# Optimization experiments

Measured on AMD Instinct MI355X. Metric: run time of the kernel, lower is better.

Reference implementation:

```python
import jax, jax.numpy as jnp
import numpy as np

N, E, M = 8192, 32768, 2048
D, H1, C = 768, 8, 768
NEG_SLOPE = 0.2


def gat_conv(x, src, dst, W, att_src, att_dst, bias, heads, out_ch):
    # PyG GATConv (eval mode, concat=True, add_self_loops already applied to src/dst)
    n = x.shape[0]
    h = (x @ W).reshape(n, heads, out_ch)                      # [N,H,C]
    a_src = jnp.einsum('nhc,hc->nh', h, att_src)               # [N,H]
    a_dst = jnp.einsum('nhc,hc->nh', h, att_dst)
    e = jax.nn.leaky_relu(a_src[src] + a_dst[dst], NEG_SLOPE)  # [E',H]
    # softmax over incoming edges of each dst node
    m = jax.ops.segment_max(e, dst, num_segments=n)
    e = jnp.exp(e - m[dst])
    denom = jax.ops.segment_sum(e, dst, num_segments=n)
    alpha = e / (denom[dst] + 1e-16)                           # [E',H]
    msg = h[src] * alpha[:, :, None]                           # [E',H,C]
    out = jax.ops.segment_sum(msg, dst, num_segments=n)        # [N,H,C]
    return out.reshape(n, heads * out_ch) + bias


def setup_inputs() -> dict:
    key = jax.random.key(0)
    ks = jax.random.split(key, 16)
    s = 0.02
    inp = {
        'x': jax.random.normal(ks[0], (N, D), jnp.float32),
        'edge_index': jax.random.randint(ks[1], (2, E), 0, N, jnp.int64),
        'mask_idx': jax.random.randint(ks[2], (M,), 0, N, jnp.int64),
        'W1': jax.random.normal(ks[3], (D, H1 * C), jnp.float32) * s,
        'att_src1': jax.random.normal(ks[4], (H1, C), jnp.float32) * s,
        'att_dst1': jax.random.normal(ks[5], (H1, C), jnp.float32) * s,
        'b1': jnp.zeros((H1 * C,), jnp.float32),
        'W2': jax.random.normal(ks[6], (H1 * C, C), jnp.float32) * s,
        'att_src2': jax.random.normal(ks[7], (1, C), jnp.float32) * s,
        'att_dst2': jax.random.normal(ks[8], (1, C), jnp.float32) * s,
        'b2': jnp.zeros((C,), jnp.float32),
        # fc: 1536 -> 768, classifier: 768 -> 2
        'fc_w': jax.random.normal(ks[9], (2 * C, C), jnp.float32) * s,
        'fc_b': jnp.zeros((C,), jnp.float32),
        'cls_w': jax.random.normal(ks[10], (C, 2), jnp.float32) * s,
        'cls_b': jnp.zeros((2,), jnp.float32),
    }
    return inp


def reference(x, edge_index, mask_idx, W1, att_src1, att_dst1, b1,
              W2, att_src2, att_dst2, b2, fc_w, fc_b, cls_w, cls_b):
    n = x.shape[0]
    loops = jnp.arange(n, dtype=edge_index.dtype)
    src = jnp.concatenate([edge_index[0], loops])   # PyG default add_self_loops
    dst = jnp.concatenate([edge_index[1], loops])
    h = gat_conv(x, src, dst, W1, att_src1, att_dst1, b1, H1, C)   # [N, 6144]
    h = jax.nn.elu(h)
    h = gat_conv(h, src, dst, W2, att_src2, att_dst2, b2, 1, C)    # [N, 768]
    x_gemb = h[mask_idx]                                           # [M, 768]
    x_emb = x[mask_idx]                                            # [M, 768]
    out = jnp.concatenate([x_gemb, x_emb], axis=1) @ fc_w + fc_b   # [M, 768]
    out = out @ cls_w + cls_b                                      # [M, 2]
    return out
```

## Files before the change

kernel.cpp:

```cpp
#include <hip/hip_runtime.h>

typedef unsigned short ushort_t;
typedef __attribute__((ext_vector_type(8))) __bf16 bf16x8;
typedef __attribute__((ext_vector_type(8))) unsigned short ushort8;
typedef __attribute__((ext_vector_type(4))) unsigned short ushort4v;
typedef __attribute__((ext_vector_type(4))) float f32x4;

#define N_NODES 8192
#define NODE_MASK 8191
#define E_EDGES 32768
#define E_TOT   40960
#define M_MASK  2048
#define D_IN    768
#define C_CH    768
#define F1      6144

typedef __attribute__((address_space(1))) const void* gas_ptr;
typedef __attribute__((address_space(3))) void* las_ptr;

__device__ __forceinline__ float bf2f(ushort_t u) {
    union { unsigned int i; float f; } v; v.i = ((unsigned int)u) << 16; return v.f;
}
__device__ __forceinline__ ushort_t f2bf(float f) {
    union { float f; unsigned int i; } v; v.f = f;
    unsigned int r = v.i + 0x7fffu + ((v.i >> 16) & 1u);
    return (ushort_t)(r >> 16);
}

__global__ void init_kernel(int* deg, int* fill, int* flags) {
    int i = blockIdx.x * 256 + threadIdx.x;
    if (i < N_NODES) { deg[i] = 0; fill[i] = 0; }
    if (i < 2) flags[i] = 0;
}
__global__ void detect_kernel(const int* __restrict__ raw, int nhalf, int* __restrict__ flag) {
    int i = blockIdx.x * 256 + threadIdx.x;
    if (i < nhalf && raw[2 * i + 1] != 0) atomicOr(flag, 1);
}
__global__ void convert_idx_kernel(const void* __restrict__ raw, int n,
                                   const int* __restrict__ flag, int* __restrict__ out) {
    int i = blockIdx.x * 256 + threadIdx.x;
    if (i >= n) return;
    int v = (*flag) ? ((const int*)raw)[i] : (int)((const long long*)raw)[i];
    out[i] = v & NODE_MASK;
}

__global__ void cvt_bf16_kernel(const float* __restrict__ in, ushort_t* __restrict__ out, int n4) {
    int i = blockIdx.x * 256 + threadIdx.x;
    if (i >= n4) return;
    f32x4 v = *(const f32x4*)(in + i * 4);
    ushort_t o0 = f2bf(v[0]), o1 = f2bf(v[1]), o2 = f2bf(v[2]), o3 = f2bf(v[3]);
    unsigned long long pk = (unsigned long long)o0 | ((unsigned long long)o1 << 16)
                          | ((unsigned long long)o2 << 32) | ((unsigned long long)o3 << 48);
    *(unsigned long long*)(out + i * 4) = pk;
}

__global__ __launch_bounds__(256) void transpose_cvt_kernel(
    const float* __restrict__ in, ushort_t* __restrict__ out, int R, int Ccols)
{
    __shared__ ushort_t tile[32][33];
    int tx = threadIdx.x & 31, ty = threadIdx.x >> 5;
    int x  = blockIdx.x * 32 + tx;
    int y0 = blockIdx.y * 32;
#pragma unroll
    for (int i = 0; i < 4; ++i)
        tile[ty + i * 8][tx] = f2bf(in[(size_t)(y0 + ty + i * 8) * Ccols + x]);
    __syncthreads();
#pragma unroll
    for (int i = 0; i < 4; ++i)
        out[(size_t)(blockIdx.x * 32 + ty + i * 8) * R + y0 + tx] = tile[tx][ty + i * 8];
}

__global__ __launch_bounds__(256) void gemm_bt_kernel(
    const ushort_t* __restrict__ A, const ushort_t* __restrict__ Bt,
    ushort_t* __restrict__ C, const float* __restrict__ bias,
    float* __restrict__ Cp,
    int M, int N, int K, int k0, int ksz)
{
    __shared__ ushort_t lsA[128 * 64];
    __shared__ ushort_t lsB[128 * 64];

    const int tid  = threadIdx.x;
    const int lane = tid & 63;
    const int wave = tid >> 6;
    const int wm = wave >> 1, wn = wave & 1;

    const int GX = gridDim.x, GY = gridDim.y;
    const int lin = blockIdx.y * GX + blockIdx.x;
    const int byg = (GY >= 8) ? (GY >> 3) : 1;
    const int xcd = lin & 7;
    const int jj  = lin >> 3;
    const int bx  = (GY >= 8) ? (jj / byg) : blockIdx.x;
    const int by  = (GY >= 8) ? (xcd * byg + (jj % byg)) : blockIdx.y;

    const f32x4 zero = {0.f, 0.f, 0.f, 0.f};
    f32x4 acc[4][4];
#pragma unroll
    for (int i = 0; i < 4; ++i)
#pragma unroll
        for (int j = 0; j < 4; ++j) acc[i][j] = zero;

    const int l8 = lane >> 3;
    const int c8 = lane & 7;
    const int q  = lane >> 4;
    const int rl = lane & 15;

    const int kbeg = k0 + blockIdx.z * ksz;
    for (int kt = kbeg; kt < kbeg + ksz; kt += 64) {
        __syncthreads();
#pragma unroll
        for (int i = 0; i < 4; ++i) {
            int rbase = wave * 32 + i * 8;
            int row   = rbase + l8;
            int gch   = c8 ^ (row & 7);
            const ushort_t* gA = A  + (size_t)(by * 128 + row) * K + kt + gch * 8;
            const ushort_t* gB = Bt + (size_t)(bx * 128 + row) * K + kt + gch * 8;
            __builtin_amdgcn_global_load_lds((gas_ptr)gA, (las_ptr)(lsA + rbase * 64), 16, 0, 0);
            __builtin_amdgcn_global_load_lds((gas_ptr)gB, (las_ptr)(lsB + rbase * 64), 16, 0, 0);
        }
        __syncthreads();
#pragma unroll
        for (int s = 0; s < 2; ++s) {
            bf16x8 af[4], bfv[4];
#pragma unroll
            for (int i = 0; i < 4; ++i) {
                int Ra = wm * 64 + i * 16 + rl;
                af[i]  = *(const bf16x8*)(lsA + Ra * 64 + (((s * 4 + q) ^ (Ra & 7)) * 8));
                int Rb = wn * 64 + i * 16 + rl;
                bfv[i] = *(const bf16x8*)(lsB + Rb * 64 + (((s * 4 + q) ^ (Rb & 7)) * 8));
            }
#pragma unroll
            for (int i = 0; i < 4; ++i)
#pragma unroll
                for (int j = 0; j < 4; ++j)
                    acc[i][j] = __builtin_amdgcn_mfma_f32_16x16x32_bf16(af[i], bfv[j], acc[i][j], 0, 0, 0);
        }
    }
    if (Cp) {
        float* Cpz = Cp + (size_t)blockIdx.z * M * N;
#pragma unroll
        for (int j = 0; j < 4; ++j) {
            int col = bx * 128 + wn * 64 + j * 16 + rl;
#pragma unroll
            for (int i = 0; i < 4; ++i)
#pragma unroll
                for (int t = 0; t < 4; ++t) {
                    int row = by * 128 + wm * 64 + i * 16 + q * 4 + t;
                    Cpz[(size_t)row * N + col] = acc[i][j][t];
                }
        }
    } else {
#pragma unroll
        for (int j = 0; j < 4; ++j) {
            int col = bx * 128 + wn * 64 + j * 16 + rl;
            float bv = bias ? bias[col] : 0.0f;
#pragma unroll
            for (int i = 0; i < 4; ++i)
#pragma unroll
                for (int t = 0; t < 4; ++t) {
                    int row = by * 128 + wm * 64 + i * 16 + q * 4 + t;
                    C[(size_t)row * N + col] = f2bf(acc[i][j][t] + bv);
                }
        }
    }
}

__global__ void indeg_kernel(const int* __restrict__ eic, int* __restrict__ deg) {
    int e = blockIdx.x * 256 + threadIdx.x;
    if (e >= E_TOT) return;
    int dst = (e < E_EDGES) ? eic[E_EDGES + e] : (e - E_EDGES);
    atomicAdd(&deg[dst], 1);
}
__global__ __launch_bounds__(256) void scan_kernel(const int* __restrict__ deg, int* __restrict__ rowptr) {
    __shared__ int part[256];
    int t = threadIdx.x;
    int local[32];
    int s = 0;
#pragma unroll
    for (int i = 0; i < 32; ++i) { local[i] = deg[t * 32 + i]; s += local[i]; }
    part[t] = s;
    __syncthreads();
    for (int off = 1; off < 256; off <<= 1) {
        int v = (t >= off) ? part[t - off] : 0;
        __syncthreads();
        part[t] += v;
        __syncthreads();
    }
    int run = (t == 0) ? 0 : part[t - 1];
#pragma unroll
    for (int i = 0; i < 32; ++i) { rowptr[t * 32 + i] = run; run += local[i]; }
    if (t == 255) rowptr[N_NODES] = run;
}
__global__ void scatter_kernel(const int* __restrict__ eic, const int* __restrict__ rowptr,
                               int* __restrict__ fill, int* __restrict__ csr_src) {
    int e = blockIdx.x * 256 + threadIdx.x;
    if (e >= E_TOT) return;
    int src, dst;
    if (e < E_EDGES) { src = eic[e]; dst = eic[E_EDGES + e]; }
    else             { src = e - E_EDGES; dst = src; }
    int pos = rowptr[dst] + atomicAdd(&fill[dst], 1);
    csr_src[pos] = src;
}

__global__ __launch_bounds__(256) void att_kernel(
    const ushort_t* __restrict__ h, const float* __restrict__ att_s,
    const float* __restrict__ att_d, float* __restrict__ a_s, float* __restrict__ a_d,
    int heads, int stride)
{
    int gid  = blockIdx.x * 4 + (threadIdx.x >> 6);
    int lane = threadIdx.x & 63;
    int n = gid / heads, hd = gid % heads;
    const ushort_t* hp = h + (size_t)n * stride + hd * C_CH;
    const float* sp = att_s + hd * C_CH;
    const float* dp = att_d + hd * C_CH;
    float s1 = 0.f, s2 = 0.f;
#pragma unroll
    for (int j = 0; j < 3; ++j) {
        int o = j * 256 + lane * 4;
        ushort4v hv = *(const ushort4v*)(hp + o);
        f32x4 sv = *(const f32x4*)(sp + o);
        f32x4 dv = *(const f32x4*)(dp + o);
#pragma unroll
        for (int k = 0; k < 4; ++k) {
            float f = bf2f(hv[k]);
            s1 += f * sv[k];
            s2 += f * dv[k];
        }
    }
#pragma unroll
    for (int off = 32; off > 0; off >>= 1) {
        s1 += __shfl_down(s1, off);
        s2 += __shfl_down(s2, off);
    }
    if (lane == 0) { a_s[gid] = s1; a_d[gid] = s2; }
}

__global__ __launch_bounds__(256) void cvtatt_kernel(
    const float* __restrict__ Cp, ushort_t* __restrict__ h2,
    const float* __restrict__ att_s, const float* __restrict__ att_d,
    float* __restrict__ a_s, float* __restrict__ a_d)
{
    __shared__ float ps[4], pd[4];
    const int n = blockIdx.x, t = threadIdx.x;
    const size_t SL = (size_t)N_NODES * 768;
    const float* row = Cp + (size_t)n * 768;
    float v0 = row[t]       + row[SL + t]       + row[2 * SL + t]       + row[3 * SL + t];
    float v1 = row[t + 256] + row[SL + t + 256] + row[2 * SL + t + 256] + row[3 * SL + t + 256];
    float v2 = row[t + 512] + row[SL + t + 512] + row[2 * SL + t + 512] + row[3 * SL + t + 512];
    h2[(size_t)n * 768 + t]       = f2bf(v0);
    h2[(size_t)n * 768 + t + 256] = f2bf(v1);
    h2[(size_t)n * 768 + t + 512] = f2bf(v2);
    float s1 = v0 * att_s[t] + v1 * att_s[t + 256] + v2 * att_s[t + 512];
    float s2 = v0 * att_d[t] + v1 * att_d[t + 256] + v2 * att_d[t + 512];
#pragma unroll
    for (int o = 32; o > 0; o >>= 1) {
        s1 += __shfl_down(s1, o);
        s2 += __shfl_down(s2, o);
    }
    if ((t & 63) == 0) { ps[t >> 6] = s1; pd[t >> 6] = s2; }
    __syncthreads();
    if (t == 0) {
        a_s[n] = ps[0] + ps[1] + ps[2] + ps[3];
        a_d[n] = pd[0] + pd[1] + pd[2] + pd[3];
    }
}

__global__ __launch_bounds__(192) void agg8_kernel(
    const ushort_t* __restrict__ h, const float* __restrict__ a_s, const float* __restrict__ a_d,
    const int* __restrict__ rowptr, const int* __restrict__ csr_src,
    const float* __restrict__ bias, ushort_t* __restrict__ out)
{
    const int n = blockIdx.x;
    const int half = blockIdx.y;
    const int tid = threadIdx.x;
    const int base = rowptr[n];
    const int deg  = rowptr[n + 1] - base;

    __shared__ float s_m[8], s_rd[8], s_adst[8];
    __shared__ int   s_src[64];
    __shared__ float s_w[64][8];

    if (tid < 8) {
        float adst = a_d[n * 8 + tid];
        float m = -1e30f;
        for (int e = 0; e < deg; ++e) {
            float scv = a_s[csr_src[base + e] * 8 + tid] + adst;
            scv = scv > 0.f ? scv : 0.2f * scv;
            m = fmaxf(m, scv);
        }
        float den = 0.f;
        for (int e = 0; e < deg; ++e) {
            float scv = a_s[csr_src[base + e] * 8 + tid] + adst;
            scv = scv > 0.f ? scv : 0.2f * scv;
            den += __expf(scv - m);
        }
        s_m[tid] = m; s_rd[tid] = 1.0f / (den + 1e-16f); s_adst[tid] = adst;
    }
    __syncthreads();

    float acc[16];
#pragma unroll
    for (int i = 0; i < 16; ++i) acc[i] = 0.f;
    const int c0   = half * 3072 + tid * 16;
    const int myhd = (half << 2) + tid / 48;

    for (int cs = 0; cs < deg; cs += 64) {
        int cnt = min(64, deg - cs);
        __syncthreads();
        for (int idx = tid; idx < cnt; idx += 192) s_src[idx] = csr_src[base + cs + idx];
        __syncthreads();
        for (int idx = tid; idx < cnt * 8; idx += 192) {
            int e = idx >> 3, hd = idx & 7;
            float scv = a_s[s_src[e] * 8 + hd] + s_adst[hd];
            scv = scv > 0.f ? scv : 0.2f * scv;
            s_w[e][hd] = __expf(scv - s_m[hd]) * s_rd[hd];
        }
        __syncthreads();
        int e = 0;
        for (; e + 3 < cnt; e += 4) {
            const ushort_t* p0 = h + (size_t)s_src[e]     * F1 + c0;
            const ushort_t* p1 = h + (size_t)s_src[e + 1] * F1 + c0;
            const ushort_t* p2 = h + (size_t)s_src[e + 2] * F1 + c0;
            const ushort_t* p3 = h + (size_t)s_src[e + 3] * F1 + c0;
            ushort8 a0 = *(const ushort8*)(p0), a1 = *(const ushort8*)(p0 + 8);
            ushort8 b0 = *(const ushort8*)(p1), b1 = *(const ushort8*)(p1 + 8);
            ushort8 c0v = *(const ushort8*)(p2), c1v = *(const ushort8*)(p2 + 8);
            ushort8 d0 = *(const ushort8*)(p3), d1 = *(const ushort8*)(p3 + 8);
            float w0 = s_w[e][myhd], w1 = s_w[e + 1][myhd];
            float w2 = s_w[e + 2][myhd], w3 = s_w[e + 3][myhd];
#pragma unroll
            for (int i = 0; i < 8; ++i) {
                acc[i]     += w0 * bf2f(a0[i]) + w1 * bf2f(b0[i]) + w2 * bf2f(c0v[i]) + w3 * bf2f(d0[i]);
                acc[8 + i] += w0 * bf2f(a1[i]) + w1 * bf2f(b1[i]) + w2 * bf2f(c1v[i]) + w3 * bf2f(d1[i]);
            }
        }
        for (; e < cnt; ++e) {
            const ushort_t* p0 = h + (size_t)s_src[e] * F1 + c0;
            ushort8 a0 = *(const ushort8*)(p0), a1 = *(const ushort8*)(p0 + 8);
            float w0 = s_w[e][myhd];
#pragma unroll
            for (int i = 0; i < 8; ++i) {
                acc[i]     += w0 * bf2f(a0[i]);
                acc[8 + i] += w0 * bf2f(a1[i]);
            }
        }
    }
#pragma unroll
    for (int i = 0; i < 16; ++i) {
        float v = acc[i] + bias[c0 + i];
        v = v > 0.f ? v : (__expf(v) - 1.0f);
        out[(size_t)n * F1 + c0 + i] = f2bf(v);
    }
}

__global__ __launch_bounds__(256) void agg1_kernel(
    const ushort_t* __restrict__ h, const float* __restrict__ a_s, const float* __restrict__ a_d,
    const int* __restrict__ rowptr, const int* __restrict__ csr_src,
    const float* __restrict__ bias, ushort_t* __restrict__ out)
{
    const int n = blockIdx.x;
    const int tid = threadIdx.x;
    const int base = rowptr[n];
    const int deg  = rowptr[n + 1] - base;
    __shared__ float s_m, s_rd, s_adst;
    __shared__ int   s_src[64];
    __shared__ float s_w[64];
    if (tid == 0) {
        float adst = a_d[n];
        float m = -1e30f;
        for (int e = 0; e < deg; ++e) {
            float scv = a_s[csr_src[base + e]] + adst;
            scv = scv > 0.f ? scv : 0.2f * scv;
            m = fmaxf(m, scv);
        }
        float den = 0.f;
        for (int e = 0; e < deg; ++e) {
            float scv = a_s[csr_src[base + e]] + adst;
            scv = scv > 0.f ? scv : 0.2f * scv;
            den += __expf(scv - m);
        }
        s_m = m; s_rd = 1.0f / (den + 1e-16f); s_adst = adst;
    }
    __syncthreads();
    float acc0 = 0.f, acc1 = 0.f, acc2 = 0.f;
    const int c0 = tid * 3;
    for (int cs = 0; cs < deg; cs += 64) {
        int cnt = min(64, deg - cs);
        __syncthreads();
        for (int idx = tid; idx < cnt; idx += 256) s_src[idx] = csr_src[base + cs + idx];
        __syncthreads();
        for (int idx = tid; idx < cnt; idx += 256) {
            float scv = a_s[s_src[idx]] + s_adst;
            scv = scv > 0.f ? scv : 0.2f * scv;
            s_w[idx] = __expf(scv - s_m) * s_rd;
        }
        __syncthreads();
        for (int e = 0; e < cnt; ++e) {
            const ushort_t* hp = h + (size_t)s_src[e] * C_CH + c0;
            float w = s_w[e];
            acc0 += w * bf2f(hp[0]);
            acc1 += w * bf2f(hp[1]);
            acc2 += w * bf2f(hp[2]);
        }
    }
    out[(size_t)n * C_CH + c0 + 0] = f2bf(acc0 + bias[c0 + 0]);
    out[(size_t)n * C_CH + c0 + 1] = f2bf(acc1 + bias[c0 + 1]);
    out[(size_t)n * C_CH + c0 + 2] = f2bf(acc2 + bias[c0 + 2]);
}

__global__ void gatherfc_kernel(const ushort_t* __restrict__ out2, const ushort_t* __restrict__ xb,
                                const int* __restrict__ maskc, ushort_t* __restrict__ Afc)
{
    int m = blockIdx.x, t = threadIdx.x;
    int mi = maskc[m];
    const ushort4v* p1 = (const ushort4v*)(out2 + (size_t)mi * 768);
    const ushort4v* p2 = (const ushort4v*)(xb   + (size_t)mi * 768);
    ushort4v* q1 = (ushort4v*)(Afc + (size_t)m * 1536);
    ushort4v* q2 = (ushort4v*)(Afc + (size_t)m * 1536 + 768);
    if (t < 192) { q1[t] = p1[t]; q2[t] = p2[t]; }
}

__global__ __launch_bounds__(256) void cls_kernel(
    const float* __restrict__ fcp, const float* __restrict__ fc_b,
    const float* __restrict__ cls_w, const float* __restrict__ cls_b,
    float* __restrict__ out)
{
    int m = blockIdx.x * 4 + (threadIdx.x >> 6);
    int lane = threadIdx.x & 63;
    const size_t SL = (size_t)M_MASK * 768;
    float a0 = 0.f, a1 = 0.f;
    const float* row = fcp + (size_t)m * 768;
    for (int i = lane; i < 768; i += 64) {
        float v = row[i] + row[SL + i] + row[2 * SL + i] + row[3 * SL + i] + fc_b[i];
        a0 += v * cls_w[i * 2 + 0];
        a1 += v * cls_w[i * 2 + 1];
    }
#pragma unroll
    for (int off = 32; off > 0; off >>= 1) {
        a0 += __shfl_down(a0, off);
        a1 += __shfl_down(a1, off);
    }
    if (lane == 0) {
        out[m * 2 + 0] = a0 + cls_b[0];
        out[m * 2 + 1] = a1 + cls_b[1];
    }
}

extern "C" void kernel_launch(void* const* d_in, const int* in_sizes, int n_in,
                              void* d_out, int out_size, void* d_ws, size_t ws_size,
                              hipStream_t stream)
{
    const float* x        = (const float*)d_in[0];
    const void*  ei_raw   = d_in[1];
    const void*  mask_raw = d_in[2];
    const float* W1       = (const float*)d_in[3];
    const float* att_src1 = (const float*)d_in[4];
    const float* att_dst1 = (const float*)d_in[5];
    const float* b1       = (const float*)d_in[6];
    const float* W2       = (const float*)d_in[7];
    const float* att_src2 = (const float*)d_in[8];
    const float* att_dst2 = (const float*)d_in[9];
    const float* b2       = (const float*)d_in[10];
    const float* fc_w     = (const float*)d_in[11];
    const float* fc_b     = (const float*)d_in[12];
    const float* cls_w    = (const float*)d_in[13];
    const float* cls_b    = (const float*)d_in[14];
    float* out = (float*)d_out;

    char* ws = (char*)d_ws;
    size_t off = 0;
    auto alloc = [&](size_t bytes) { char* p = ws + off; off = (off + bytes + 255) & ~(size_t)255; return p; };
    int*   flags  = (int*)alloc(2 * 4);
    int*   eic    = (int*)alloc((size_t)2 * E_EDGES * 4);
    int*   maskc  = (int*)alloc((size_t)M_MASK * 4);
    int*   deg    = (int*)alloc(N_NODES * 4);
    int*   fill   = (int*)alloc(N_NODES * 4);
    int*   rowptr = (int*)alloc((N_NODES + 1) * 4);
    int*   csr    = (int*)alloc(E_TOT * 4);
    float* a_s1   = (float*)alloc((size_t)N_NODES * 8 * 4);
    float* a_d1   = (float*)alloc((size_t)N_NODES * 8 * 4);
    float* a_s2   = (float*)alloc((size_t)N_NODES * 4);
    float* a_d2   = (float*)alloc((size_t)N_NODES * 4);
    ushort_t* W1t  = (ushort_t*)alloc((size_t)D_IN * F1 * 2);
    ushort_t* W2t  = (ushort_t*)alloc((size_t)F1 * C_CH * 2);
    ushort_t* fcwt = (ushort_t*)alloc((size_t)1536 * 768 * 2);
    ushort_t* xb   = (ushort_t*)alloc((size_t)N_NODES * D_IN * 2);
    char* region1 = alloc((size_t)N_NODES * F1 * 2);
    char* region2 = alloc((size_t)N_NODES * F1 * 2);
    ushort_t* h1  = (ushort_t*)region1;
    float*    Cp  = (float*)region1;
    float*    fcp = (float*)region1;
    ushort_t* out1 = (ushort_t*)region2;
    ushort_t* out2 = (ushort_t*)region2;
    ushort_t* h2   = (ushort_t*)(region2 + (16u << 20));
    ushort_t* Afc  = (ushort_t*)(region2 + (32u << 20));

    init_kernel<<<N_NODES / 256, 256, 0, stream>>>(deg, fill, flags);
    detect_kernel<<<(E_EDGES + 255) / 256, 256, 0, stream>>>((const int*)ei_raw, E_EDGES, &flags[0]);
    detect_kernel<<<(M_MASK / 2 + 255) / 256, 256, 0, stream>>>((const int*)mask_raw, M_MASK / 2, &flags[1]);
    convert_idx_kernel<<<(2 * E_EDGES + 255) / 256, 256, 0, stream>>>(ei_raw, 2 * E_EDGES, &flags[0], eic);
    convert_idx_kernel<<<(M_MASK + 255) / 256, 256, 0, stream>>>(mask_raw, M_MASK, &flags[1], maskc);
    indeg_kernel<<<E_TOT / 256, 256, 0, stream>>>(eic, deg);
    scan_kernel<<<1, 256, 0, stream>>>(deg, rowptr);
    scatter_kernel<<<E_TOT / 256, 256, 0, stream>>>(eic, rowptr, fill, csr);

    cvt_bf16_kernel<<<(N_NODES * D_IN / 4 + 255) / 256, 256, 0, stream>>>(x, xb, N_NODES * D_IN / 4);
    transpose_cvt_kernel<<<dim3(F1 / 32, D_IN / 32), 256, 0, stream>>>(W1, W1t, D_IN, F1);
    transpose_cvt_kernel<<<dim3(C_CH / 32, F1 / 32), 256, 0, stream>>>(W2, W2t, F1, C_CH);
    transpose_cvt_kernel<<<dim3(768 / 32, 1536 / 32), 256, 0, stream>>>(fc_w, fcwt, 1536, 768);

    gemm_bt_kernel<<<dim3(F1 / 128, N_NODES / 128), 256, 0, stream>>>(
        xb, W1t, h1, nullptr, nullptr, N_NODES, F1, D_IN, 0, D_IN);
    att_kernel<<<(N_NODES * 8) / 4, 256, 0, stream>>>(h1, att_src1, att_dst1, a_s1, a_d1, 8, F1);
    agg8_kernel<<<dim3(N_NODES, 2), 192, 0, stream>>>(h1, a_s1, a_d1, rowptr, csr, b1, out1);

    gemm_bt_kernel<<<dim3(C_CH / 128, N_NODES / 128, 4), 256, 0, stream>>>(
        out1, W2t, nullptr, nullptr, Cp, N_NODES, C_CH, F1, 0, F1 / 4);
    cvtatt_kernel<<<N_NODES, 256, 0, stream>>>(Cp, h2, att_src2, att_dst2, a_s2, a_d2);
    agg1_kernel<<<N_NODES, 256, 0, stream>>>(h2, a_s2, a_d2, rowptr, csr, b2, out2);

    gatherfc_kernel<<<M_MASK, 256, 0, stream>>>(out2, xb, maskc, Afc);
    gemm_bt_kernel<<<dim3(768 / 128, M_MASK / 128, 4), 256, 0, stream>>>(
        Afc, fcwt, nullptr, nullptr, fcp, M_MASK, 768, 1536, 0, 1536 / 4);
    cls_kernel<<<M_MASK / 4, 256, 0, stream>>>(fcp, fc_b, cls_w, cls_b, out);
}
```

Measured before the change: 553.3 us.

## Fuse layer-1 attention dot products into GEMM epilogue; bf16 split-K partials

The layer-1 GEMM epilogue now computes per-tile partial dot products of the accumulators with att_src/att_dst, reduces them across lanes and writes them to small per-slot buffers. A tiny reduction kernel sums the 12 slots per head, which replaces the att_kernel that re-read the full 8192x6144 bf16 h1. Separately, the layer-2 split-K GEMM now writes its partials as bf16 rather than fp32, halving the traffic that cvtatt reads. The bf16 partials lose some precision before summation, and the epilogue adds shuffle work to the first GEMM.

```diff
diff --git a/kernel.cpp b/kernel.cpp
--- a/kernel.cpp
+++ b/kernel.cpp
@@ -74,7 +74,9 @@
     const ushort_t* __restrict__ A, const ushort_t* __restrict__ Bt,
     ushort_t* __restrict__ C, const float* __restrict__ bias,
     float* __restrict__ Cp,
-    int M, int N, int K, int k0, int ksz)
+    const float* __restrict__ att_s, const float* __restrict__ att_d,
+    float* __restrict__ Ps, float* __restrict__ Pd, int bx_per_head,
+    int M, int N, int K, int ksz)
 {
     __shared__ ushort_t lsA[128 * 64];
     __shared__ ushort_t lsB[128 * 64];
@@ -104,7 +106,7 @@
     const int q  = lane >> 4;
     const int rl = lane & 15;
 
-    const int kbeg = k0 + blockIdx.z * ksz;
+    const int kbeg = blockIdx.z * ksz;
     for (int kt = kbeg; kt < kbeg + ksz; kt += 64) {
         __syncthreads();
 #pragma unroll
@@ -149,6 +151,7 @@
                 }
         }
     } else {
+        ushort_t* Cz = C + (size_t)blockIdx.z * M * N;
 #pragma unroll
         for (int j = 0; j < 4; ++j) {
             int col = bx * 128 + wn * 64 + j * 16 + rl;
@@ -158,10 +161,59 @@
 #pragma unroll
                 for (int t = 0; t < 4; ++t) {
                     int row = by * 128 + wm * 64 + i * 16 + q * 4 + t;
-                    C[(size_t)row * N + col] = f2bf(acc[i][j][t] + bv);
+                    Cz[(size_t)row * N + col] = f2bf(acc[i][j][t] + bv);
                 }
         }
     }
+    if (bx_per_head > 0) {
+        const int head = bx / bx_per_head;
+        const int slot = (bx % bx_per_head) * 2 + wn;
+        const int colh = (bx % bx_per_head) * 128 + wn * 64 + rl;
+        float as_[4], ad_[4];
+#pragma unroll
+        for (int j = 0; j < 4; ++j) {
+            as_[j] = att_s[head * 768 + colh + j * 16];
+            ad_[j] = att_d[head * 768 + colh + j * 16];
+        }
+        float* ps = Ps + (size_t)(head * 12 + slot) * M;
+        float* pd = Pd + (size_t)(head * 12 + slot) * M;
+#pragma unroll
+        for (int i = 0; i < 4; ++i)
+#pragma unroll
+            for (int t = 0; t < 4; ++t) {
+                float p1 = 0.f, p2 = 0.f;
+#pragma unroll
+                for (int j = 0; j < 4; ++j) {
+                    p1 += acc[i][j][t] * as_[j];
+                    p2 += acc[i][j][t] * ad_[j];
+                }
+#pragma unroll
+                for (int o = 1; o < 16; o <<= 1) {
+                    p1 += __shfl_xor(p1, o);
+                    p2 += __shfl_xor(p2, o);
+                }
+                if (rl == 0) {
+                    int row = by * 128 + wm * 64 + i * 16 + q * 4 + t;
+                    ps[row] = p1;
+                    pd[row] = p2;
+                }
+            }
+    }
+}
+
+__global__ void att1red_kernel(const float* __restrict__ Ps, const float* __restrict__ Pd,
+                               float* __restrict__ a_s, float* __restrict__ a_d)
+{
+    int gid = blockIdx.x * 256 + threadIdx.x;
+    int h = gid >> 13, n = gid & 8191;
+    float s = 0.f, d = 0.f;
+#pragma unroll
+    for (int slot = 0; slot < 12; ++slot) {
+        s += Ps[((size_t)(h * 12 + slot) << 13) + n];
+        d += Pd[((size_t)(h * 12 + slot) << 13) + n];
+    }
+    a_s[n * 8 + h] = s;
+    a_d[n * 8 + h] = d;
 }
 
 __global__ void indeg_kernel(const int* __restrict__ eic, int* __restrict__ deg) {
@@ -201,51 +253,18 @@
     csr_src[pos] = src;
 }
 
-__global__ __launch_bounds__(256) void att_kernel(
-    const ushort_t* __restrict__ h, const float* __restrict__ att_s,
-    const float* __restrict__ att_d, float* __restrict__ a_s, float* __restrict__ a_d,
-    int heads, int stride)
-{
-    int gid  = blockIdx.x * 4 + (threadIdx.x >> 6);
-    int lane = threadIdx.x & 63;
-    int n = gid / heads, hd = gid % heads;
-    const ushort_t* hp = h + (size_t)n * stride + hd * C_CH;
-    const float* sp = att_s + hd * C_CH;
-    const float* dp = att_d + hd * C_CH;
-    float s1 = 0.f, s2 = 0.f;
-#pragma unroll
-    for (int j = 0; j < 3; ++j) {
-        int o = j * 256 + lane * 4;
-        ushort4v hv = *(const ushort4v*)(hp + o);
-        f32x4 sv = *(const f32x4*)(sp + o);
-        f32x4 dv = *(const f32x4*)(dp + o);
-#pragma unroll
-        for (int k = 0; k < 4; ++k) {
-            float f = bf2f(hv[k]);
-            s1 += f * sv[k];
-            s2 += f * dv[k];
-        }
-    }
-#pragma unroll
-    for (int off = 32; off > 0; off >>= 1) {
-        s1 += __shfl_down(s1, off);
-        s2 += __shfl_down(s2, off);
-    }
-    if (lane == 0) { a_s[gid] = s1; a_d[gid] = s2; }
-}
-
 __global__ __launch_bounds__(256) void cvtatt_kernel(
-    const float* __restrict__ Cp, ushort_t* __restrict__ h2,
+    const ushort_t* __restrict__ Cb, ushort_t* __restrict__ h2,
     const float* __restrict__ att_s, const float* __restrict__ att_d,
     float* __restrict__ a_s, float* __restrict__ a_d)
 {
     __shared__ float ps[4], pd[4];
     const int n = blockIdx.x, t = threadIdx.x;
     const size_t SL = (size_t)N_NODES * 768;
-    const float* row = Cp + (size_t)n * 768;
-    float v0 = row[t]       + row[SL + t]       + row[2 * SL + t]       + row[3 * SL + t];
-    float v1 = row[t + 256] + row[SL + t + 256] + row[2 * SL + t + 256] + row[3 * SL + t + 256];
-    float v2 = row[t + 512] + row[SL + t + 512] + row[2 * SL + t + 512] + row[3 * SL + t + 512];
+    const ushort_t* row = Cb + (size_t)n * 768;
+    float v0 = bf2f(row[t])       + bf2f(row[SL + t])       + bf2f(row[2 * SL + t])       + bf2f(row[3 * SL + t]);
+    float v1 = bf2f(row[t + 256]) + bf2f(row[SL + t + 256]) + bf2f(row[2 * SL + t + 256]) + bf2f(row[3 * SL + t + 256]);
+    float v2 = bf2f(row[t + 512]) + bf2f(row[SL + t + 512]) + bf2f(row[2 * SL + t + 512]) + bf2f(row[3 * SL + t + 512]);
     h2[(size_t)n * 768 + t]       = f2bf(v0);
     h2[(size_t)n * 768 + t + 256] = f2bf(v1);
     h2[(size_t)n * 768 + t + 512] = f2bf(v2);
@@ -480,6 +499,8 @@
     float* a_d1   = (float*)alloc((size_t)N_NODES * 8 * 4);
     float* a_s2   = (float*)alloc((size_t)N_NODES * 4);
     float* a_d2   = (float*)alloc((size_t)N_NODES * 4);
+    float* Ps     = (float*)alloc((size_t)8 * 12 * N_NODES * 4);
+    float* Pd     = (float*)alloc((size_t)8 * 12 * N_NODES * 4);
     ushort_t* W1t  = (ushort_t*)alloc((size_t)D_IN * F1 * 2);
     ushort_t* W2t  = (ushort_t*)alloc((size_t)F1 * C_CH * 2);
     ushort_t* fcwt = (ushort_t*)alloc((size_t)1536 * 768 * 2);
@@ -487,7 +508,7 @@
     char* region1 = alloc((size_t)N_NODES * F1 * 2);
     char* region2 = alloc((size_t)N_NODES * F1 * 2);
     ushort_t* h1  = (ushort_t*)region1;
-    float*    Cp  = (float*)region1;
+    ushort_t* Cb  = (ushort_t*)region1;
     float*    fcp = (float*)region1;
     ushort_t* out1 = (ushort_t*)region2;
     ushort_t* out2 = (ushort_t*)region2;
@@ -509,17 +530,20 @@
     transpose_cvt_kernel<<<dim3(768 / 32, 1536 / 32), 256, 0, stream>>>(fc_w, fcwt, 1536, 768);
 
     gemm_bt_kernel<<<dim3(F1 / 128, N_NODES / 128), 256, 0, stream>>>(
-        xb, W1t, h1, nullptr, nullptr, N_NODES, F1, D_IN, 0, D_IN);
-    att_kernel<<<(N_NODES * 8) / 4, 256, 0, stream>>>(h1, att_src1, att_dst1, a_s1, a_d1, 8, F1);
+        xb, W1t, h1, nullptr, nullptr, att_src1, att_dst1, Ps, Pd, 6,
+        N_NODES, F1, D_IN, D_IN);
+    att1red_kernel<<<(N_NODES * 8) / 256, 256, 0, stream>>>(Ps, Pd, a_s1, a_d1);
     agg8_kernel<<<dim3(N_NODES, 2), 192, 0, stream>>>(h1, a_s1, a_d1, rowptr, csr, b1, out1);
 
     gemm_bt_kernel<<<dim3(C_CH / 128, N_NODES / 128, 4), 256, 0, stream>>>(
-        out1, W2t, nullptr, nullptr, Cp, N_NODES, C_CH, F1, 0, F1 / 4);
-    cvtatt_kernel<<<N_NODES, 256, 0, stream>>>(Cp, h2, att_src2, att_dst2, a_s2, a_d2);
+        out1, W2t, Cb, nullptr, nullptr, nullptr, nullptr, nullptr, nullptr, 0,
+        N_NODES, C_CH, F1, F1 / 4);
+    cvtatt_kernel<<<N_NODES, 256, 0, stream>>>(Cb, h2, att_src2, att_dst2, a_s2, a_d2);
     agg1_kernel<<<N_NODES, 256, 0, stream>>>(h2, a_s2, a_d2, rowptr, csr, b2, out2);
 
     gatherfc_kernel<<<M_MASK, 256, 0, stream>>>(out2, xb, maskc, Afc);
     gemm_bt_kernel<<<dim3(768 / 128, M_MASK / 128, 4), 256, 0, stream>>>(
-        Afc, fcwt, nullptr, nullptr, fcp, M_MASK, 768, 1536, 0, 1536 / 4);
+        Afc, fcwt, nullptr, nullptr, fcp, nullptr, nullptr, nullptr, nullptr, 0,
+        M_MASK, 768, 1536, 1536 / 4);
     cls_kernel<<<M_MASK / 4, 256, 0, stream>>>(fcp, fc_b, cls_w, cls_b, out);
 }
```

Measured after the change: 551.6 us. About the same (-0.3%).
